# Kernel tuning notes

Hardware: AMD Instinct MI355X
Metric: run time of the kernel (lower is better)

## Reference

```python
import jax, jax.numpy as jnp
import numpy as np

C_I, C_T, NUM_HEADS = 128, 256, 8
EPS = 1e-5

def conv3d1(x, W, b):
    # 1x1x1 conv: x (b,c,D,H,W), W (o,c), b (o,)
    return jnp.einsum('oc,bcdhw->bodhw', W, x) + b[None, :, None, None, None]

def conv1d1(x, W, b):
    # kernel_size=1 conv: x (b,c,l), W (o,c), b (o,)
    return jnp.einsum('oc,bcl->bol', W, x) + b[None, :, None]

def inorm3d(x):
    # InstanceNorm3d(affine=False): normalize over spatial dims, biased var
    m = jnp.mean(x, axis=(2, 3, 4), keepdims=True)
    v = jnp.var(x, axis=(2, 3, 4), keepdims=True)
    return (x - m) * jax.lax.rsqrt(v + EPS)

def setup_inputs() -> dict:
    key = jax.random.key(0)
    ks = jax.random.split(key, 20)
    B, D, H, W, L = 2, 48, 48, 48, 20
    s = 0.05
    inp = {
        'img_in': jax.random.normal(ks[0], (B, C_I, D, H, W), jnp.float32),
        'lang_in': jax.random.normal(ks[1], (B, C_T, L), jnp.float32),
        'Wq': jax.random.normal(ks[2], (C_I, C_I), jnp.float32) * s,
        'bq': jnp.zeros((C_I,), jnp.float32),
        'Wk': jax.random.normal(ks[3], (C_I, C_T), jnp.float32) * s,
        'bk': jnp.zeros((C_I,), jnp.float32),
        'Wv': jax.random.normal(ks[4], (C_I, C_T), jnp.float32) * s,
        'bv': jnp.zeros((C_I,), jnp.float32),
        'Wpw': jax.random.normal(ks[5], (C_I, C_I), jnp.float32) * s,
        'bpw': jnp.zeros((C_I,), jnp.float32),
        'Wpi': jax.random.normal(ks[6], (C_I, C_I), jnp.float32) * s,
        'bpi': jnp.zeros((C_I,), jnp.float32),
        'Wpo': jax.random.normal(ks[7], (C_I, C_I), jnp.float32) * s,
        'bpo': jnp.zeros((C_I,), jnp.float32),
        'Wg1': jax.random.normal(ks[8], (C_I, C_I), jnp.float32) * s,
        'bg1': jnp.zeros((C_I,), jnp.float32),
        'Wg2': jax.random.normal(ks[9], (C_I, C_I), jnp.float32) * s,
        'bg2': jnp.zeros((C_I,), jnp.float32),
    }
    return inp

def reference(img_in, lang_in, Wq, bq, Wk, bk, Wv, bv, Wpw, bpw, Wpi, bpi,
              Wpo, bpo, Wg1, bg1, Wg2, bg2):
    b = img_in.shape[0]
    d = int(np.prod(img_in.shape[-3:]))
    l = lang_in.shape[-1]
    hd = C_I // NUM_HEADS
    # lang_mask=None path -> all-ones mask (additive term is zero but kept faithful)
    mask = jnp.ones((b, 1, l), img_in.dtype)

    # query: conv3d(1x1)+InstanceNorm -> (b, heads, d, hd)
    q = inorm3d(conv3d1(img_in, Wq, bq)).reshape(b, C_I, d)
    q = q.transpose(0, 2, 1).reshape(b, d, NUM_HEADS, hd).transpose(0, 2, 1, 3)
    # key/value: conv1d(k=1) masked -> (b, heads, hd, l)
    k = (conv1d1(lang_in, Wk, bk) * mask).reshape(b, NUM_HEADS, hd, l)
    v = (conv1d1(lang_in, Wv, bv) * mask).reshape(b, NUM_HEADS, hd, l)

    scale = (C_I / NUM_HEADS) ** (-0.5)
    sim = jnp.einsum('bhdc,bhcl->bhdl', q, k) * scale
    sim = sim + (10000.0 * mask[:, :, None, :] - 10000.0)  # (b,1,1,l) broadcast
    attn = jax.nn.softmax(sim, axis=-1)
    x = jnp.einsum('bhdl,bhcl->bhdc', attn, v)              # (b,heads,d,hd)
    x = x.transpose(0, 2, 1, 3).reshape(b, d, C_I)
    # faithful to torch .permute(0,2,1).permute(0,2,1).view_as(img_in):
    # reshape (b, d, c_i) flat buffer into (b, c_i, D, H, W)
    x_img = x.reshape(img_in.shape)

    skip = inorm3d(conv3d1(img_in, Wpi, bpi))
    weight = inorm3d(conv3d1(x_img, Wpw, bpw))
    out = jax.nn.relu(conv3d1(skip * weight, Wpo, bpo))
    gate = jnp.tanh(conv3d1(jax.nn.relu(conv3d1(out, Wg1, bg1)), Wg2, bg2))
    return out * gate
```

## Files before the change

kernel.cpp:

```cpp
#include <hip/hip_runtime.h>
#include <cstdint>
#include <cstddef>

#define PSP 110592
#define NCH 128
#define NB  2
#define CPW 68
#define TPB 4
static constexpr float EPSV = 1e-5f;

typedef short bf16x8 __attribute__((ext_vector_type(8)));
typedef float f32x4  __attribute__((ext_vector_type(4)));

static __device__ __forceinline__ short f2bf(float f) {
    uint32_t u = __builtin_bit_cast(uint32_t, f);
    u += 0x7FFF + ((u >> 16) & 1);
    return (short)(u >> 16);
}
static __device__ __forceinline__ float bf2f(short s) {
    uint32_t u = ((uint32_t)(uint16_t)s) << 16;
    return __builtin_bit_cast(float, u);
}
static __device__ __forceinline__ float bfLO(uint32_t w) { return bf2f((short)(w & 0xffff)); }
static __device__ __forceinline__ float bfHI(uint32_t w) { return bf2f((short)(w >> 16)); }
static __device__ __forceinline__ uint32_t pk2f(float lo, float hi) {
    return (uint32_t)(uint16_t)f2bf(lo) | ((uint32_t)(uint16_t)f2bf(hi) << 16);
}
static __device__ __forceinline__ uint32_t pk2s(short lo, short hi) {
    return (uint32_t)(uint16_t)lo | ((uint32_t)(uint16_t)hi << 16);
}
static __device__ __forceinline__ int swzb(int p) {
    return (((p & 7) ^ ((p >> 3) & 7)) << 4);
}

__global__ __launch_bounds__(256) void kv_kernel(
    const float* __restrict__ lang,
    const float* __restrict__ Wk, const float* __restrict__ bk,
    const float* __restrict__ Wv, const float* __restrict__ bv,
    float* __restrict__ kout, float* __restrict__ vout)
{
    int gid = blockIdx.x * 256 + threadIdx.x;
    int sel = gid / 5120;
    int r   = gid % 5120;
    int b   = r / 2560;
    int o   = (r % 2560) / 20;
    int l   = r % 20;
    const float* W  = sel ? Wv : Wk;
    const float* bb = sel ? bv : bk;
    const float* lg = lang + b * 256 * 20 + l;
    float acc = bb[o];
    #pragma unroll 8
    for (int c = 0; c < 256; ++c)
        acc = fmaf(W[o * 256 + c], lg[c * 20], acc);
    (sel ? vout : kout)[b * 2560 + o * 20 + l] = acc;
}

__global__ __launch_bounds__(256) void wprep_kernel(
    const float* __restrict__ w0, const float* __restrict__ w1,
    const float* __restrict__ w2, const float* __restrict__ w3,
    const float* __restrict__ w4, const float* __restrict__ w5,
    short* __restrict__ wt)
{
    const int m = blockIdx.x >> 4, s = blockIdx.x & 15;
    const float* src = w0;
    if (m == 1) src = w1; else if (m == 2) src = w2; else if (m == 3) src = w3;
    else if (m == 4) src = w4; else if (m == 5) src = w5;
    short* dst = wt + m * NCH * NCH;
    const int i0 = s * 1024 + threadIdx.x * 4;
    f32x4 v = *(const f32x4*)(src + i0);
    *(uint2*)(dst + i0) = make_uint2(pk2f(v[0], v[1]) ,
                                     pk2f(v[2], v[3]));
}

__global__ __launch_bounds__(256) void knprep_kernel(
    const float* __restrict__ qs, const float* __restrict__ qs2,
    const float* __restrict__ kbuf,
    float* __restrict__ knb, float* __restrict__ cbb)
{
    __shared__ float mq[128], rqs[128], knl[2560];
    const int t = threadIdx.x, b = blockIdx.x;
    if (t < 128) {
        float m = qs[b * 128 + t] * (1.0f / PSP);
        float v = qs2[b * 128 + t] * (1.0f / PSP) - m * m;
        mq[t] = m;
        rqs[t] = rsqrtf(v + EPSV) * 0.25f;
    }
    __syncthreads();
    for (int e = t; e < 2560; e += 256) {
        int c = e / 20;
        float kv = rqs[c] * kbuf[b * 2560 + e];
        knl[e] = kv;
        knb[b * 2560 + e] = kv;
    }
    __syncthreads();
    if (t < 160) {
        int h = t / 20, l = t % 20;
        float s = 0.0f;
        #pragma unroll
        for (int i = 0; i < 16; ++i)
            s = fmaf(mq[h * 16 + i], knl[(h * 16 + i) * 20 + l], s);
        cbb[b * 160 + t] = s;
    }
}

struct PackW { uint32_t lo[8], hi[8]; };

static __device__ __forceinline__ void ldpack_f32(const float* src, PackW& w) {
    const int t = threadIdx.x;
    const float* s = src + (size_t)(4 * (t >> 3)) * PSP + (t & 7) * 8;
    f32x4 r0a = *(const f32x4*)s,             r0b = *(const f32x4*)(s + 4);
    f32x4 r1a = *(const f32x4*)(s + PSP),     r1b = *(const f32x4*)(s + PSP + 4);
    f32x4 r2a = *(const f32x4*)(s + 2 * PSP), r2b = *(const f32x4*)(s + 2 * PSP + 4);
    f32x4 r3a = *(const f32x4*)(s + 3 * PSP), r3b = *(const f32x4*)(s + 3 * PSP + 4);
    #pragma unroll
    for (int j = 0; j < 4; ++j) {
        w.lo[j]     = pk2f(r0a[j], r1a[j]);
        w.lo[4 + j] = pk2f(r0b[j], r1b[j]);
        w.hi[j]     = pk2f(r2a[j], r3a[j]);
        w.hi[4 + j] = pk2f(r2b[j], r3b[j]);
    }
}
static __device__ __forceinline__ void ldpack_b16(const short* src, PackW& w) {
    const int t = threadIdx.x;
    const short* s = src + (size_t)(4 * (t >> 3)) * PSP + (t & 7) * 8;
    bf16x8 r0 = *(const bf16x8*)s;
    bf16x8 r1 = *(const bf16x8*)(s + PSP);
    bf16x8 r2 = *(const bf16x8*)(s + 2 * PSP);
    bf16x8 r3 = *(const bf16x8*)(s + 3 * PSP);
    #pragma unroll
    for (int j = 0; j < 8; ++j) { w.lo[j] = pk2s(r0[j], r1[j]); w.hi[j] = pk2s(r2[j], r3[j]); }
}
static __device__ __forceinline__ void ldpack_g4(const short* skip, const short* wgt,
        const float nm[4][NCH], PackW& w) {
    const int t = threadIdx.x;
    const int c = 4 * (t >> 3), p0 = (t & 7) * 8;
    const short* s = skip + (size_t)c * PSP + p0;
    const short* g = wgt  + (size_t)c * PSP + p0;
    bf16x8 s0 = *(const bf16x8*)s,             s1 = *(const bf16x8*)(s + PSP);
    bf16x8 s2 = *(const bf16x8*)(s + 2 * PSP), s3 = *(const bf16x8*)(s + 3 * PSP);
    bf16x8 g0 = *(const bf16x8*)g,             g1 = *(const bf16x8*)(g + PSP);
    bf16x8 g2 = *(const bf16x8*)(g + 2 * PSP), g3 = *(const bf16x8*)(g + 3 * PSP);
    float mA[4], rA[4], mB[4], rB[4];
    #pragma unroll
    for (int r = 0; r < 4; ++r) {
        mA[r] = nm[0][c + r]; rA[r] = nm[1][c + r];
        mB[r] = nm[2][c + r]; rB[r] = nm[3][c + r];
    }
    #pragma unroll
    for (int j = 0; j < 8; ++j) {
        float v0 = ((bf2f(s0[j]) - mA[0]) * rA[0]) * ((bf2f(g0[j]) - mB[0]) * rB[0]);
        float v1 = ((bf2f(s1[j]) - mA[1]) * rA[1]) * ((bf2f(g1[j]) - mB[1]) * rB[1]);
        float v2 = ((bf2f(s2[j]) - mA[2]) * rA[2]) * ((bf2f(g2[j]) - mB[2]) * rB[2]);
        float v3 = ((bf2f(s3[j]) - mA[3]) * rA[3]) * ((bf2f(g3[j]) - mB[3]) * rB[3]);
        w.lo[j] = pk2f(v0, v1);
        w.hi[j] = pk2f(v2, v3);
    }
}
static __device__ __forceinline__ void stage(char* STGb, const PackW& w) {
    const int t = threadIdx.x;
    const int c8 = (t >> 3) * 8, p0 = (t & 7) * 8;
    #pragma unroll
    for (int j = 0; j < 8; ++j) {
        int byte = (p0 + j) * 256 + c8;
        byte ^= ((j ^ (t & 7)) << 4);
        *(uint2*)(STGb + byte) = make_uint2(w.lo[j], w.hi[j]);
    }
}

static __device__ __forceinline__ void load_afrag16(const short* __restrict__ W16,
                                                    int wid, int lane, bf16x8 af[2][4]) {
    const int orow = wid * 32 + (lane & 15);
    const int cb   = (lane >> 4) * 8;
    #pragma unroll
    for (int mt = 0; mt < 2; ++mt)
        #pragma unroll
        for (int kt = 0; kt < 4; ++kt)
            af[mt][kt] = *(const bf16x8*)(W16 + (size_t)(orow + mt * 16) * NCH + kt * 32 + cb);
}

static __device__ __forceinline__ void run_mfmaX(const char* STGb, const bf16x8 af[2][4],
                                                 f32x4 acc[2][4], int lane) {
    const int l15 = lane & 15, kh = lane >> 4;
    #pragma unroll
    for (int nt = 0; nt < 4; ++nt) {
        const int p = nt * 16 + l15;
        const int sw = swzb(p);
        bf16x8 bf[4];
        #pragma unroll
        for (int kt = 0; kt < 4; ++kt)
            bf[kt] = *(const bf16x8*)(STGb + ((p * 256 + kt * 64 + kh * 16) ^ sw));
        #pragma unroll
        for (int kt = 0; kt < 4; ++kt) {
            acc[0][nt] = __builtin_amdgcn_mfma_f32_16x16x32_bf16(af[0][kt], bf[kt], acc[0][nt], 0, 0, 0);
            acc[1][nt] = __builtin_amdgcn_mfma_f32_16x16x32_bf16(af[1][kt], bf[kt], acc[1][nt], 0, 0, 0);
        }
    }
}
static __device__ __forceinline__ void zero_acc(f32x4 acc[2][4]) {
    #pragma unroll
    for (int m = 0; m < 2; ++m)
        #pragma unroll
        for (int n = 0; n < 4; ++n) acc[m][n] = (f32x4)0.0f;
}
static __device__ __forceinline__ void write_LCp(uint32_t* LCp, const f32x4 acc[2][4],
                                                 int wid, int lane) {
    const int l15 = lane & 15, og = wid * 32 + (lane >> 4) * 4;
    #pragma unroll
    for (int mt = 0; mt < 2; ++mt)
        #pragma unroll
        for (int nt = 0; nt < 4; ++nt) {
            const int o2 = (og >> 1) + mt * 8, p = nt * 16 + l15;
            f32x4 a = acc[mt][nt];
            LCp[o2 * CPW + p]       = pk2f(a[0], a[1]);
            LCp[(o2 + 1) * CPW + p] = pk2f(a[2], a[3]);
        }
}
template<bool RELU, bool STATS>
static __device__ __forceinline__ void epi2(const uint32_t* LCp, const float* __restrict__ bias,
        short* __restrict__ dst, float sS[4], float sQ[4])
{
    const int t = threadIdx.x;
    #pragma unroll
    for (int r = 0; r < 4; ++r) {
        const int u = r * 256 + t, o = u >> 3, ch = u & 7, hi = o & 1;
        const float bia = bias[o];
        const uint32_t* src = LCp + (o >> 1) * CPW + ch * 8;
        uint4 wa = *(const uint4*)src;
        uint4 wb = *(const uint4*)(src + 4);
        uint32_t ww[8] = {wa.x, wa.y, wa.z, wa.w, wb.x, wb.y, wb.z, wb.w};
        float v[8];
        #pragma unroll
        for (int j = 0; j < 8; ++j) v[j] = (hi ? bfHI(ww[j]) : bfLO(ww[j])) + bia;
        if (RELU) {
            #pragma unroll
            for (int j = 0; j < 8; ++j) v[j] = fmaxf(v[j], 0.0f);
        }
        bf16x8 s8;
        #pragma unroll
        for (int j = 0; j < 8; ++j) s8[j] = f2bf(v[j]);
        *(bf16x8*)(dst + (size_t)o * PSP + ch * 8) = s8;
        if (STATS) {
            float s = 0.0f, q = 0.0f;
            #pragma unroll
            for (int j = 0; j < 8; ++j) { s += v[j]; q += v[j] * v[j]; }
            sS[r] += s; sQ[r] += q;
        }
    }
}
static __device__ __forceinline__ void flush_stats(const float sS[4], const float sQ[4],
        float* __restrict__ s_sum, float* __restrict__ s_sq)
{
    const int t = threadIdx.x;
    #pragma unroll
    for (int r = 0; r < 4; ++r) {
        float s = sS[r], q = sQ[r];
        s += __shfl_xor(s, 1); q += __shfl_xor(q, 1);
        s += __shfl_xor(s, 2); q += __shfl_xor(q, 2);
        s += __shfl_xor(s, 4); q += __shfl_xor(q, 4);
        if ((t & 7) == 0) {
            atomicAdd(&s_sum[r * 32 + (t >> 3)], s);
            atomicAdd(&s_sq [r * 32 + (t >> 3)], q);
        }
    }
}

__global__ __launch_bounds__(256) void g12_kernel(
    const float* __restrict__ img, const short* __restrict__ w16,
    const float* __restrict__ bq, const float* __restrict__ bpi,
    short* __restrict__ qout, short* __restrict__ sout,
    float* __restrict__ qs, float* __restrict__ qs2,
    float* __restrict__ ss, float* __restrict__ ss2)
{
    __shared__ __align__(16) char STGb[16384];
    __shared__ __align__(16) uint32_t LCp[64 * CPW];

    const int t = threadIdx.x, lane = t & 63, wid = t >> 6;
    const int b = blockIdx.y;
    const size_t bbase = (size_t)b * NCH * PSP;
    const int pbase = blockIdx.x * (64 * TPB);
    const int sb = b * NCH;

    bf16x8 afq[2][4], afp[2][4];
    load_afrag16(w16, wid, lane, afq);
    load_afrag16(w16 + NCH * NCH, wid, lane, afp);

    float qS[4] = {0, 0, 0, 0}, qQ[4] = {0, 0, 0, 0};
    float sS[4] = {0, 0, 0, 0}, sQ[4] = {0, 0, 0, 0};

    PackW w;
    ldpack_f32(img + bbase + pbase, w);

    for (int i = 0; i < TPB; ++i) {
        const int pblk = pbase + i * 64;
        stage(STGb, w);
        __syncthreads();
        if (i + 1 < TPB) ldpack_f32(img + bbase + pblk + 64, w);
        f32x4 acc[2][4];
        zero_acc(acc);
        run_mfmaX(STGb, afq, acc, lane);
        write_LCp(LCp, acc, wid, lane);
        __syncthreads();
        epi2<false, true>(LCp, bq, qout + bbase + pblk, qS, qQ);
        zero_acc(acc);
        run_mfmaX(STGb, afp, acc, lane);
        __syncthreads();
        write_LCp(LCp, acc, wid, lane);
        __syncthreads();
        epi2<false, true>(LCp, bpi, sout + bbase + pblk, sS, sQ);
    }
    flush_stats(qS, qQ, qs + sb, qs2 + sb);
    flush_stats(sS, sQ, ss + sb, ss2 + sb);
}

__global__ __launch_bounds__(256) void g3_kernel(
    const short* __restrict__ x, const short* __restrict__ w16,
    const float* __restrict__ bpw, short* __restrict__ wout,
    float* __restrict__ wsu, float* __restrict__ ws2)
{
    __shared__ __align__(16) char STGb[16384];
    __shared__ __align__(16) uint32_t LCp[64 * CPW];

    const int t = threadIdx.x, lane = t & 63, wid = t >> 6;
    const int b = blockIdx.y;
    const size_t bbase = (size_t)b * NCH * PSP;
    const int pbase = blockIdx.x * (64 * TPB);
    const int sb = b * NCH;

    bf16x8 af[2][4];
    load_afrag16(w16, wid, lane, af);
    float wS[4] = {0, 0, 0, 0}, wQ[4] = {0, 0, 0, 0};

    PackW w;
    ldpack_b16(x + bbase + pbase, w);

    for (int i = 0; i < TPB; ++i) {
        const int pblk = pbase + i * 64;
        stage(STGb, w);
        __syncthreads();
        if (i + 1 < TPB) ldpack_b16(x + bbase + pblk + 64, w);
        f32x4 acc[2][4];
        zero_acc(acc);
        run_mfmaX(STGb, af, acc, lane);
        write_LCp(LCp, acc, wid, lane);
        __syncthreads();
        epi2<false, true>(LCp, bpw, wout + bbase + pblk, wS, wQ);
    }
    flush_stats(wS, wQ, wsu + sb, ws2 + sb);
}

__global__ __launch_bounds__(256) void g4_kernel(
    const short* __restrict__ skip, const short* __restrict__ wgt,
    const float* __restrict__ sA, const float* __restrict__ sA2,
    const float* __restrict__ sB, const float* __restrict__ sB2,
    const short* __restrict__ w16, const float* __restrict__ bpo,
    short* __restrict__ outp)
{
    __shared__ __align__(16) char STGb[16384];
    __shared__ __align__(16) uint32_t LCp[64 * CPW];
    __shared__ float nm[4][NCH];

    const int t = threadIdx.x, lane = t & 63, wid = t >> 6;
    const int b = blockIdx.y;
    const size_t bbase = (size_t)b * NCH * PSP;
    const int pbase = blockIdx.x * (64 * TPB);

    if (t < NCH) {
        float m = sA[b * NCH + t] * (1.0f / PSP);
        float v = sA2[b * NCH + t] * (1.0f / PSP) - m * m;
        nm[0][t] = m; nm[1][t] = rsqrtf(v + EPSV);
    } else {
        int c = t - NCH;
        float m = sB[b * NCH + c] * (1.0f / PSP);
        float v = sB2[b * NCH + c] * (1.0f / PSP) - m * m;
        nm[2][c] = m; nm[3][c] = rsqrtf(v + EPSV);
    }
    bf16x8 af[2][4];
    load_afrag16(w16, wid, lane, af);
    __syncthreads();

    PackW w;
    ldpack_g4(skip + bbase + pbase, wgt + bbase + pbase, nm, w);
    float dS[4], dQ[4];

    for (int i = 0; i < TPB; ++i) {
        const int pblk = pbase + i * 64;
        stage(STGb, w);
        __syncthreads();
        if (i + 1 < TPB)
            ldpack_g4(skip + bbase + pblk + 64, wgt + bbase + pblk + 64, nm, w);
        f32x4 acc[2][4];
        zero_acc(acc);
        run_mfmaX(STGb, af, acc, lane);
        write_LCp(LCp, acc, wid, lane);
        __syncthreads();
        epi2<true, false>(LCp, bpo, outp + bbase + pblk, dS, dQ);
    }
}

__global__ __launch_bounds__(256) void g56_kernel(
    const short* __restrict__ outb, const short* __restrict__ w16g1,
    const float* __restrict__ bg1, const short* __restrict__ w16g2,
    const float* __restrict__ bg2, float* __restrict__ fin)
{
    __shared__ __align__(16) char STGb[16384];
    __shared__ __align__(16) char RTL[64 * CPW * 4];

    const int t = threadIdx.x, lane = t & 63, wid = t >> 6;
    const int b = blockIdx.y;
    const size_t bbase = (size_t)b * NCH * PSP;
    const int pbase = blockIdx.x * (64 * TPB);

    bf16x8 af1[2][4], af2[2][4];
    load_afrag16(w16g1, wid, lane, af1);
    load_afrag16(w16g2, wid, lane, af2);

    float bg1v[2][4];
    {
        const int og = wid * 32 + (lane >> 4) * 4;
        #pragma unroll
        for (int mt = 0; mt < 2; ++mt)
            #pragma unroll
            for (int r = 0; r < 4; ++r) bg1v[mt][r] = bg1[og + mt * 16 + r];
    }

    PackW w;
    ldpack_b16(outb + bbase + pbase, w);

    for (int i = 0; i < TPB; ++i) {
        const int pblk = pbase + i * 64;
        stage(STGb, w);
        __syncthreads();
        if (i + 1 < TPB) ldpack_b16(outb + bbase + pblk + 64, w);
        f32x4 acc[2][4];
        zero_acc(acc);
        run_mfmaX(STGb, af1, acc, lane);
        {
            const int l15 = lane & 15, og = wid * 32 + (lane >> 4) * 4;
            #pragma unroll
            for (int mt = 0; mt < 2; ++mt)
                #pragma unroll
                for (int nt = 0; nt < 4; ++nt) {
                    const int o = og + mt * 16, p = nt * 16 + l15;
                    const int sw = swzb(p);
                    f32x4 a = acc[mt][nt];
                    float z0 = fmaxf(a[0] + bg1v[mt][0], 0.0f);
                    float z1 = fmaxf(a[1] + bg1v[mt][1], 0.0f);
                    float z2 = fmaxf(a[2] + bg1v[mt][2], 0.0f);
                    float z3 = fmaxf(a[3] + bg1v[mt][3], 0.0f);
                    *(uint32_t*)(RTL + ((p * 256 + o * 2) ^ sw))     = pk2f(z0, z1);
                    *(uint32_t*)(RTL + ((p * 256 + o * 2 + 4) ^ sw)) = pk2f(z2, z3);
                }
        }
        __syncthreads();
        zero_acc(acc);
        run_mfmaX(RTL, af2, acc, lane);
        __syncthreads();
        write_LCp((uint32_t*)RTL, acc, wid, lane);
        __syncthreads();
        {
            const uint32_t* LCp = (const uint32_t*)RTL;
            float* dst = fin + bbase + pblk;
            #pragma unroll
            for (int r = 0; r < 4; ++r) {
                const int u = r * 256 + t, o2 = u >> 4, ch = u & 15;
                const float b0 = bg2[2 * o2], b1 = bg2[2 * o2 + 1];
                uint4 lc = *(const uint4*)(LCp + o2 * CPW + ch * 4);
                uint32_t lw[4] = {lc.x, lc.y, lc.z, lc.w};
                f32x4 oA, oB;
                #pragma unroll
                for (int j = 0; j < 4; ++j) {
                    const int p = ch * 4 + j;
                    uint32_t mw = *(const uint32_t*)(STGb + ((p * 256 + o2 * 4) ^ swzb(p)));
                    oA[j] = bfLO(mw) * tanhf(bfLO(lw[j]) + b0);
                    oB[j] = bfHI(mw) * tanhf(bfHI(lw[j]) + b1);
                }
                *(f32x4*)(dst + (size_t)(2 * o2) * PSP + ch * 4)     = oA;
                *(f32x4*)(dst + (size_t)(2 * o2 + 1) * PSP + ch * 4) = oB;
            }
        }
        __syncthreads();
    }
}

__global__ __launch_bounds__(256) void attn3_kernel(
    const short* __restrict__ qpre, const float* __restrict__ knb,
    const float* __restrict__ cbb, const float* __restrict__ vbuf,
    short* __restrict__ xout)
{
    __shared__ __align__(16) uint32_t QX[64 * 65];
    __shared__ float KN[2560], VV[2560], CB[160];

    const int t = threadIdx.x;
    const int b = blockIdx.y;
    const int pblk = blockIdx.x * 64;
    const size_t bbase = (size_t)b * NCH * PSP;

    {
        const float* kn = knb + b * 2560;
        const float* vv = vbuf + b * 2560;
        #pragma unroll
        for (int e = t; e < 2560; e += 256) { KN[e] = kn[e]; VV[e] = vv[e]; }
        if (t < 160) CB[t] = cbb[b * 160 + t];
    }
    {
        const int c2 = t >> 2, p0 = (t & 3) * 16;
        const short* s0 = qpre + bbase + (size_t)(2 * c2) * PSP + pblk + p0;
        bf16x8 a0 = *(const bf16x8*)s0,         a1 = *(const bf16x8*)(s0 + 8);
        bf16x8 b0 = *(const bf16x8*)(s0 + PSP), b1 = *(const bf16x8*)(s0 + PSP + 8);
        uint32_t w[16];
        #pragma unroll
        for (int k = 0; k < 8; ++k) { w[k] = pk2s(a0[k], b0[k]); w[8 + k] = pk2s(a1[k], b1[k]); }
        uint32_t* base = QX + c2 * 65 + p0;
        #pragma unroll
        for (int k = 0; k < 8; ++k) *(uint2*)(base + 2 * k) = make_uint2(w[2 * k], w[2 * k + 1]);
    }
    __syncthreads();

    const int p = t & 63, h0 = t >> 6;
    uint32_t qw[16];
    #pragma unroll
    for (int i = 0; i < 8; ++i) {
        qw[i]     = QX[(h0 * 8 + i) * 65 + p];
        qw[8 + i] = QX[((h0 + 4) * 8 + i) * 65 + p];
    }
    __syncthreads();

    #pragma unroll 1
    for (int hh = 0; hh < 2; ++hh) {
        const int h = h0 + hh * 4;
        const int c0 = h * 16;
        float sim[20];
        #pragma unroll
        for (int l = 0; l < 20; ++l) sim[l] = -CB[h * 20 + l];
        #pragma unroll
        for (int i = 0; i < 8; ++i) {
            const uint32_t w = qw[hh * 8 + i];
            const float qlo = bfLO(w), qhi = bfHI(w);
            const float* k0 = KN + (c0 + 2 * i) * 20;
            #pragma unroll
            for (int l = 0; l < 20; ++l)
                sim[l] = fmaf(qlo, k0[l], fmaf(qhi, k0[20 + l], sim[l]));
        }
        float mx = sim[0];
        #pragma unroll
        for (int l = 1; l < 20; ++l) mx = fmaxf(mx, sim[l]);
        float se = 0.0f;
        #pragma unroll
        for (int l = 0; l < 20; ++l) { float e = __expf(sim[l] - mx); sim[l] = e; se += e; }
        const float inv = 1.0f / se;
        #pragma unroll
        for (int i = 0; i < 8; ++i) {
            const float* v0 = VV + (c0 + 2 * i) * 20;
            float x0 = 0.0f, x1 = 0.0f;
            #pragma unroll
            for (int l = 0; l < 20; ++l) {
                x0 = fmaf(sim[l], v0[l], x0);
                x1 = fmaf(sim[l], v0[20 + l], x1);
            }
            QX[p * 65 + h * 8 + i] = pk2f(x0 * inv, x1 * inv);
        }
    }
    __syncthreads();

    {
        const int lane = t & 63, w = t >> 6;
        uint32_t* gdst = (uint32_t*)(xout + bbase + (size_t)pblk * NCH);
        #pragma unroll
        for (int j = 0; j < 4; ++j) {
            const int pp = w * 4 + j * 16 + (lane >> 4);
            const int cw = (lane & 15) * 4;
            const uint32_t* s = QX + pp * 65 + cw;
            *(uint4*)(gdst + pp * 64 + cw) = make_uint4(s[0], s[1], s[2], s[3]);
        }
    }
}

extern "C" void kernel_launch(void* const* d_in, const int* in_sizes, int n_in,
                              void* d_out, int out_size, void* d_ws, size_t ws_size,
                              hipStream_t stream)
{
    const float* img  = (const float*)d_in[0];
    const float* lang = (const float*)d_in[1];
    const float* Wq   = (const float*)d_in[2];
    const float* bq   = (const float*)d_in[3];
    const float* Wk   = (const float*)d_in[4];
    const float* bk   = (const float*)d_in[5];
    const float* Wv   = (const float*)d_in[6];
    const float* bv   = (const float*)d_in[7];
    const float* Wpw  = (const float*)d_in[8];
    const float* bpw  = (const float*)d_in[9];
    const float* Wpi  = (const float*)d_in[10];
    const float* bpi  = (const float*)d_in[11];
    const float* Wpo  = (const float*)d_in[12];
    const float* bpo  = (const float*)d_in[13];
    const float* Wg1  = (const float*)d_in[14];
    const float* bg1  = (const float*)d_in[15];
    const float* Wg2  = (const float*)d_in[16];
    const float* bg2  = (const float*)d_in[17];
    float* outp = (float*)d_out;

    const size_t N = (size_t)NB * NCH * PSP;
    const size_t needed = 3 * N * sizeof(short) + 6 * NCH * NCH * sizeof(short)
                        + (3 * 2 * 2560 + 2 * 160 + 6 * 256) * sizeof(float);
    if (ws_size < needed) return;

    short* bufA = (short*)d_ws;
    short* bufB = bufA + N;
    short* bufC = bufB + N;
    short* wt16 = bufC + N;
    float* kbuf = (float*)(wt16 + 6 * NCH * NCH);
    float* vbuf = kbuf + 2 * 2560;
    float* knb  = vbuf + 2 * 2560;
    float* cbb  = knb + 2 * 2560;
    float* st   = cbb + 2 * 160;
    float* qs   = st;
    float* qs2  = st + 256;
    float* ss   = st + 512;
    float* ss2  = st + 768;
    float* wsu  = st + 1024;
    float* ws2  = st + 1280;

    hipMemsetAsync(st, 0, 6 * 256 * sizeof(float), stream);
    kv_kernel<<<dim3(40), dim3(256), 0, stream>>>(lang, Wk, bk, Wv, bv, kbuf, vbuf);
    wprep_kernel<<<dim3(96), dim3(256), 0, stream>>>(Wq, Wpi, Wpw, Wpo, Wg1, Wg2, wt16);

    const dim3 gg(PSP / (64 * TPB), NB), gb(256);

    g12_kernel<<<gg, gb, 0, stream>>>(img, wt16, bq, bpi, bufA, bufC, qs, qs2, ss, ss2);
    knprep_kernel<<<dim3(NB), dim3(256), 0, stream>>>(qs, qs2, kbuf, knb, cbb);
    attn3_kernel<<<dim3(PSP / 64, NB), gb, 0, stream>>>(bufA, knb, cbb, vbuf, bufB);
    g3_kernel<<<gg, gb, 0, stream>>>(bufB, wt16 + 2 * NCH * NCH, bpw, bufA, wsu, ws2);
    g4_kernel<<<gg, gb, 0, stream>>>(bufC, bufA, ss, ss2, wsu, ws2,
                                     wt16 + 3 * NCH * NCH, bpo, bufB);
    g56_kernel<<<gg, gb, 0, stream>>>(bufB, wt16 + 4 * NCH * NCH, bg1,
                                      wt16 + 5 * NCH * NCH, bg2, outp);
}
```

Baseline: 322.2 us.

## Store Q position-major, simplify attention kernel, repack loads, use hardware bf16 conversion

The q projection is now written in position-major (pixel x channel) layout straight from the g12 epilogue through a swizzled LDS tile, with stats computed in registers. The attention kernel then reads each pixel's 128-channel row directly, one thread per pixel, and drops the LDS transpose. Input packing switches to 8-channel by 4-position loads with byte-perm packing and uint4 LDS stores, bf16 conversion uses the packed intrinsic, and the norm is folded into scale/shift FMAs. TPB is halved, which doubles the block count and repeats weight-fragment loads more often.

New measurement: 430.8 us. +33.7%, slower.

```diff
diff --git a/kernel.cpp b/kernel.cpp
--- a/kernel.cpp
+++ b/kernel.cpp
@@ -1,4 +1,5 @@
 #include <hip/hip_runtime.h>
+#include <hip/hip_bf16.h>
 #include <cstdint>
 #include <cstddef>
 
@@ -6,28 +7,23 @@
 #define NCH 128
 #define NB  2
 #define CPW 68
-#define TPB 4
+#define TPB 2
 static constexpr float EPSV = 1e-5f;
 
 typedef short bf16x8 __attribute__((ext_vector_type(8)));
 typedef float f32x4  __attribute__((ext_vector_type(4)));
 
-static __device__ __forceinline__ short f2bf(float f) {
-    uint32_t u = __builtin_bit_cast(uint32_t, f);
-    u += 0x7FFF + ((u >> 16) & 1);
-    return (short)(u >> 16);
-}
-static __device__ __forceinline__ float bf2f(short s) {
-    uint32_t u = ((uint32_t)(uint16_t)s) << 16;
-    return __builtin_bit_cast(float, u);
-}
-static __device__ __forceinline__ float bfLO(uint32_t w) { return bf2f((short)(w & 0xffff)); }
-static __device__ __forceinline__ float bfHI(uint32_t w) { return bf2f((short)(w >> 16)); }
-static __device__ __forceinline__ uint32_t pk2f(float lo, float hi) {
-    return (uint32_t)(uint16_t)f2bf(lo) | ((uint32_t)(uint16_t)f2bf(hi) << 16);
-}
-static __device__ __forceinline__ uint32_t pk2s(short lo, short hi) {
-    return (uint32_t)(uint16_t)lo | ((uint32_t)(uint16_t)hi << 16);
+static __device__ __forceinline__ uint32_t cvtpk(float lo, float hi) {
+    __hip_bfloat162 h = __float22bfloat162_rn(make_float2(lo, hi));
+    uint32_t u;
+    __builtin_memcpy(&u, &h, 4);
+    return u;
+}
+static __device__ __forceinline__ float bfLO(uint32_t w) {
+    return __builtin_bit_cast(float, w << 16);
+}
+static __device__ __forceinline__ float bfHI(uint32_t w) {
+    return __builtin_bit_cast(float, w & 0xffff0000u);
 }
 static __device__ __forceinline__ int swzb(int p) {
     return (((p & 7) ^ ((p >> 3) & 7)) << 4);
@@ -68,8 +64,7 @@
     short* dst = wt + m * NCH * NCH;
     const int i0 = s * 1024 + threadIdx.x * 4;
     f32x4 v = *(const f32x4*)(src + i0);
-    *(uint2*)(dst + i0) = make_uint2(pk2f(v[0], v[1]) ,
-                                     pk2f(v[2], v[3]));
+    *(uint2*)(dst + i0) = make_uint2(cvtpk(v[0], v[1]), cvtpk(v[2], v[3]));
 }
 
 __global__ __launch_bounds__(256) void knprep_kernel(
@@ -103,67 +98,82 @@
     }
 }
 
-struct PackW { uint32_t lo[8], hi[8]; };
-
-static __device__ __forceinline__ void ldpack_f32(const float* src, PackW& w) {
+struct PackR { uint32_t r[4][4]; };
+
+static __device__ __forceinline__ void ldpack_f32(const float* src, PackR& w) {
     const int t = threadIdx.x;
-    const float* s = src + (size_t)(4 * (t >> 3)) * PSP + (t & 7) * 8;
-    f32x4 r0a = *(const f32x4*)s,             r0b = *(const f32x4*)(s + 4);
-    f32x4 r1a = *(const f32x4*)(s + PSP),     r1b = *(const f32x4*)(s + PSP + 4);
-    f32x4 r2a = *(const f32x4*)(s + 2 * PSP), r2b = *(const f32x4*)(s + 2 * PSP + 4);
-    f32x4 r3a = *(const f32x4*)(s + 3 * PSP), r3b = *(const f32x4*)(s + 3 * PSP + 4);
+    const float* s = src + (size_t)((t >> 4) * 8) * PSP + (t & 15) * 4;
+    f32x4 F[8];
+    #pragma unroll
+    for (int r = 0; r < 8; ++r) F[r] = *(const f32x4*)(s + (size_t)r * PSP);
+    #pragma unroll
+    for (int j = 0; j < 4; ++j)
+        #pragma unroll
+        for (int k = 0; k < 4; ++k)
+            w.r[j][k] = cvtpk(F[2 * k][j], F[2 * k + 1][j]);
+}
+static __device__ __forceinline__ void ldpack_b16(const short* src, PackR& w) {
+    const int t = threadIdx.x;
+    const short* s = src + (size_t)((t >> 4) * 8) * PSP + (t & 15) * 4;
+    uint2 L[8];
+    #pragma unroll
+    for (int r = 0; r < 8; ++r) L[r] = *(const uint2*)(s + (size_t)r * PSP);
     #pragma unroll
     for (int j = 0; j < 4; ++j) {
-        w.lo[j]     = pk2f(r0a[j], r1a[j]);
-        w.lo[4 + j] = pk2f(r0b[j], r1b[j]);
-        w.hi[j]     = pk2f(r2a[j], r3a[j]);
-        w.hi[4 + j] = pk2f(r2b[j], r3b[j]);
-    }
-}
-static __device__ __forceinline__ void ldpack_b16(const short* src, PackW& w) {
+        const uint32_t sel = (j & 1) ? 0x07060302u : 0x05040100u;
+        #pragma unroll
+        for (int k = 0; k < 4; ++k) {
+            uint32_t wa = (j & 2) ? L[2 * k].y : L[2 * k].x;
+            uint32_t wb = (j & 2) ? L[2 * k + 1].y : L[2 * k + 1].x;
+            w.r[j][k] = __builtin_amdgcn_perm(wb, wa, sel);
+        }
+    }
+}
+static __device__ __forceinline__ void ldpack_g4(const short* skip, const short* wgt,
+        const float nm[4][NCH], PackR& w) {
     const int t = threadIdx.x;
-    const short* s = src + (size_t)(4 * (t >> 3)) * PSP + (t & 7) * 8;
-    bf16x8 r0 = *(const bf16x8*)s;
-    bf16x8 r1 = *(const bf16x8*)(s + PSP);
-    bf16x8 r2 = *(const bf16x8*)(s + 2 * PSP);
-    bf16x8 r3 = *(const bf16x8*)(s + 3 * PSP);
-    #pragma unroll
-    for (int j = 0; j < 8; ++j) { w.lo[j] = pk2s(r0[j], r1[j]); w.hi[j] = pk2s(r2[j], r3[j]); }
-}
-static __device__ __forceinline__ void ldpack_g4(const short* skip, const short* wgt,
-        const float nm[4][NCH], PackW& w) {
+    const int c0 = (t >> 4) * 8, p0 = (t & 15) * 4;
+    const short* s = skip + (size_t)c0 * PSP + p0;
+    const short* g = wgt  + (size_t)c0 * PSP + p0;
+    uint2 LS[8], LG[8];
+    #pragma unroll
+    for (int r = 0; r < 8; ++r) {
+        LS[r] = *(const uint2*)(s + (size_t)r * PSP);
+        LG[r] = *(const uint2*)(g + (size_t)r * PSP);
+    }
+    float rA[8], tA[8], rB[8], tB[8];
+    #pragma unroll
+    for (int r = 0; r < 8; ++r) {
+        rA[r] = nm[0][c0 + r]; tA[r] = nm[1][c0 + r];
+        rB[r] = nm[2][c0 + r]; tB[r] = nm[3][c0 + r];
+    }
+    #pragma unroll
+    for (int j = 0; j < 4; ++j) {
+        #pragma unroll
+        for (int k = 0; k < 4; ++k) {
+            uint32_t wa = (j & 2) ? LS[2 * k].y : LS[2 * k].x;
+            uint32_t wb = (j & 2) ? LS[2 * k + 1].y : LS[2 * k + 1].x;
+            uint32_t ga = (j & 2) ? LG[2 * k].y : LG[2 * k].x;
+            uint32_t gb = (j & 2) ? LG[2 * k + 1].y : LG[2 * k + 1].x;
+            float s0 = (j & 1) ? bfHI(wa) : bfLO(wa);
+            float s1 = (j & 1) ? bfHI(wb) : bfLO(wb);
+            float g0 = (j & 1) ? bfHI(ga) : bfLO(ga);
+            float g1 = (j & 1) ? bfHI(gb) : bfLO(gb);
+            float v0 = fmaf(s0, rA[2 * k], tA[2 * k]) * fmaf(g0, rB[2 * k], tB[2 * k]);
+            float v1 = fmaf(s1, rA[2 * k + 1], tA[2 * k + 1]) * fmaf(g1, rB[2 * k + 1], tB[2 * k + 1]);
+            w.r[j][k] = cvtpk(v0, v1);
+        }
+    }
+}
+static __device__ __forceinline__ void stage(char* STGb, const PackR& w) {
     const int t = threadIdx.x;
-    const int c = 4 * (t >> 3), p0 = (t & 7) * 8;
-    const short* s = skip + (size_t)c * PSP + p0;
-    const short* g = wgt  + (size_t)c * PSP + p0;
-    bf16x8 s0 = *(const bf16x8*)s,             s1 = *(const bf16x8*)(s + PSP);
-    bf16x8 s2 = *(const bf16x8*)(s + 2 * PSP), s3 = *(const bf16x8*)(s + 3 * PSP);
-    bf16x8 g0 = *(const bf16x8*)g,             g1 = *(const bf16x8*)(g + PSP);
-    bf16x8 g2 = *(const bf16x8*)(g + 2 * PSP), g3 = *(const bf16x8*)(g + 3 * PSP);
-    float mA[4], rA[4], mB[4], rB[4];
-    #pragma unroll
-    for (int r = 0; r < 4; ++r) {
-        mA[r] = nm[0][c + r]; rA[r] = nm[1][c + r];
-        mB[r] = nm[2][c + r]; rB[r] = nm[3][c + r];
-    }
-    #pragma unroll
-    for (int j = 0; j < 8; ++j) {
-        float v0 = ((bf2f(s0[j]) - mA[0]) * rA[0]) * ((bf2f(g0[j]) - mB[0]) * rB[0]);
-        float v1 = ((bf2f(s1[j]) - mA[1]) * rA[1]) * ((bf2f(g1[j]) - mB[1]) * rB[1]);
-        float v2 = ((bf2f(s2[j]) - mA[2]) * rA[2]) * ((bf2f(g2[j]) - mB[2]) * rB[2]);
-        float v3 = ((bf2f(s3[j]) - mA[3]) * rA[3]) * ((bf2f(g3[j]) - mB[3]) * rB[3]);
-        w.lo[j] = pk2f(v0, v1);
-        w.hi[j] = pk2f(v2, v3);
-    }
-}
-static __device__ __forceinline__ void stage(char* STGb, const PackW& w) {
-    const int t = threadIdx.x;
-    const int c8 = (t >> 3) * 8, p0 = (t & 7) * 8;
-    #pragma unroll
-    for (int j = 0; j < 8; ++j) {
-        int byte = (p0 + j) * 256 + c8;
-        byte ^= ((j ^ (t & 7)) << 4);
-        *(uint2*)(STGb + byte) = make_uint2(w.lo[j], w.hi[j]);
+    const int cB = (t >> 4) * 16, p0 = (t & 15) * 4;
+    #pragma unroll
+    for (int j = 0; j < 4; ++j) {
+        const int p = p0 + j;
+        int byte = p * 256 + cB;
+        byte ^= swzb(p);
+        *(uint4*)(STGb + byte) = make_uint4(w.r[j][0], w.r[j][1], w.r[j][2], w.r[j][3]);
     }
 }
 
@@ -177,7 +187,6 @@
         for (int kt = 0; kt < 4; ++kt)
             af[mt][kt] = *(const bf16x8*)(W16 + (size_t)(orow + mt * 16) * NCH + kt * 32 + cb);
 }
-
 static __device__ __forceinline__ void run_mfmaX(const char* STGb, const bf16x8 af[2][4],
                                                  f32x4 acc[2][4], int lane) {
     const int l15 = lane & 15, kh = lane >> 4;
@@ -211,8 +220,8 @@
         for (int nt = 0; nt < 4; ++nt) {
             const int o2 = (og >> 1) + mt * 8, p = nt * 16 + l15;
             f32x4 a = acc[mt][nt];
-            LCp[o2 * CPW + p]       = pk2f(a[0], a[1]);
-            LCp[(o2 + 1) * CPW + p] = pk2f(a[2], a[3]);
+            LCp[o2 * CPW + p]       = cvtpk(a[0], a[1]);
+            LCp[(o2 + 1) * CPW + p] = cvtpk(a[2], a[3]);
         }
 }
 template<bool RELU, bool STATS>
@@ -235,10 +244,9 @@
             #pragma unroll
             for (int j = 0; j < 8; ++j) v[j] = fmaxf(v[j], 0.0f);
         }
-        bf16x8 s8;
-        #pragma unroll
-        for (int j = 0; j < 8; ++j) s8[j] = f2bf(v[j]);
-        *(bf16x8*)(dst + (size_t)o * PSP + ch * 8) = s8;
+        *(uint4*)(dst + (size_t)o * PSP + ch * 8) =
+            make_uint4(cvtpk(v[0], v[1]), cvtpk(v[2], v[3]),
+                       cvtpk(v[4], v[5]), cvtpk(v[6], v[7]));
         if (STATS) {
             float s = 0.0f, q = 0.0f;
             #pragma unroll
@@ -267,9 +275,101 @@
 __global__ __launch_bounds__(256) void g12_kernel(
     const float* __restrict__ img, const short* __restrict__ w16,
     const float* __restrict__ bq, const float* __restrict__ bpi,
-    short* __restrict__ qout, short* __restrict__ sout,
+    short* __restrict__ qpm, short* __restrict__ sout,
     float* __restrict__ qs, float* __restrict__ qs2,
     float* __restrict__ ss, float* __restrict__ ss2)
+{
+    __shared__ __align__(16) char STGb[16384];
+    __shared__ __align__(16) char LC[64 * CPW * 4];
+
+    const int t = threadIdx.x, lane = t & 63, wid = t >> 6;
+    const int b = blockIdx.y;
+    const size_t bbase = (size_t)b * NCH * PSP;
+    const size_t bpos  = (size_t)b * PSP;
+    const int pbase = blockIdx.x * (64 * TPB);
+    const int sb = b * NCH;
+
+    bf16x8 afq[2][4], afp[2][4];
+    load_afrag16(w16, wid, lane, afq);
+    load_afrag16(w16 + NCH * NCH, wid, lane, afp);
+
+    const int og0 = wid * 32 + (lane >> 4) * 4;
+    float bqv[2][4];
+    #pragma unroll
+    for (int mt = 0; mt < 2; ++mt)
+        #pragma unroll
+        for (int r = 0; r < 4; ++r) bqv[mt][r] = bq[og0 + mt * 16 + r];
+
+    float qS[2][4] = {{0,0,0,0},{0,0,0,0}}, qQ[2][4] = {{0,0,0,0},{0,0,0,0}};
+    float sS[4] = {0,0,0,0}, sQ[4] = {0,0,0,0};
+
+    PackR w;
+    ldpack_f32(img + bbase + pbase, w);
+
+    for (int i = 0; i < TPB; ++i) {
+        const int pblk = pbase + i * 64;
+        stage(STGb, w);
+        __syncthreads();
+        if (i + 1 < TPB) ldpack_f32(img + bbase + pblk + 64, w);
+        f32x4 acc[2][4];
+        zero_acc(acc);
+        run_mfmaX(STGb, afq, acc, lane);
+        {
+            const int l15 = lane & 15;
+            #pragma unroll
+            for (int mt = 0; mt < 2; ++mt)
+                #pragma unroll
+                for (int nt = 0; nt < 4; ++nt) {
+                    const int o = og0 + mt * 16, p = nt * 16 + l15, sw = swzb(p);
+                    f32x4 a = acc[mt][nt];
+                    float v0 = a[0] + bqv[mt][0], v1 = a[1] + bqv[mt][1];
+                    float v2 = a[2] + bqv[mt][2], v3 = a[3] + bqv[mt][3];
+                    *(uint32_t*)(LC + ((p * 256 + o * 2)     ^ sw)) = cvtpk(v0, v1);
+                    *(uint32_t*)(LC + ((p * 256 + o * 2 + 4) ^ sw)) = cvtpk(v2, v3);
+                    qS[mt][0] += v0; qS[mt][1] += v1; qS[mt][2] += v2; qS[mt][3] += v3;
+                    qQ[mt][0] += v0 * v0; qQ[mt][1] += v1 * v1;
+                    qQ[mt][2] += v2 * v2; qQ[mt][3] += v3 * v3;
+                }
+        }
+        __syncthreads();
+        {
+            const int p = t >> 2, cq = t & 3;
+            const int sw = swzb(p);
+            short* qdst = qpm + (size_t)(bpos + pblk + p) * 128 + cq * 32;
+            #pragma unroll
+            for (int k = 0; k < 4; ++k) {
+                uint4 d = *(const uint4*)(LC + ((p * 256 + cq * 64 + k * 16) ^ sw));
+                *(uint4*)(qdst + k * 8) = d;
+            }
+        }
+        zero_acc(acc);
+        run_mfmaX(STGb, afp, acc, lane);
+        __syncthreads();
+        write_LCp((uint32_t*)LC, acc, wid, lane);
+        __syncthreads();
+        epi2<false, true>((const uint32_t*)LC, bpi, sout + bbase + pblk, sS, sQ);
+    }
+    #pragma unroll
+    for (int mt = 0; mt < 2; ++mt)
+        #pragma unroll
+        for (int r = 0; r < 4; ++r) {
+            float s = qS[mt][r], q = qQ[mt][r];
+            s += __shfl_xor(s, 1); q += __shfl_xor(q, 1);
+            s += __shfl_xor(s, 2); q += __shfl_xor(q, 2);
+            s += __shfl_xor(s, 4); q += __shfl_xor(q, 4);
+            s += __shfl_xor(s, 8); q += __shfl_xor(q, 8);
+            if ((lane & 15) == 0) {
+                atomicAdd(&qs [sb + og0 + mt * 16 + r], s);
+                atomicAdd(&qs2[sb + og0 + mt * 16 + r], q);
+            }
+        }
+    flush_stats(sS, sQ, ss + sb, ss2 + sb);
+}
+
+__global__ __launch_bounds__(256) void g3_kernel(
+    const short* __restrict__ x, const short* __restrict__ w16,
+    const float* __restrict__ bpw, short* __restrict__ wout,
+    float* __restrict__ wsu, float* __restrict__ ws2)
 {
     __shared__ __align__(16) char STGb[16384];
     __shared__ __align__(16) uint32_t LCp[64 * CPW];
@@ -280,57 +380,11 @@
     const int pbase = blockIdx.x * (64 * TPB);
     const int sb = b * NCH;
 
-    bf16x8 afq[2][4], afp[2][4];
-    load_afrag16(w16, wid, lane, afq);
-    load_afrag16(w16 + NCH * NCH, wid, lane, afp);
-
-    float qS[4] = {0, 0, 0, 0}, qQ[4] = {0, 0, 0, 0};
-    float sS[4] = {0, 0, 0, 0}, sQ[4] = {0, 0, 0, 0};
-
-    PackW w;
-    ldpack_f32(img + bbase + pbase, w);
-
-    for (int i = 0; i < TPB; ++i) {
-        const int pblk = pbase + i * 64;
-        stage(STGb, w);
-        __syncthreads();
-        if (i + 1 < TPB) ldpack_f32(img + bbase + pblk + 64, w);
-        f32x4 acc[2][4];
-        zero_acc(acc);
-        run_mfmaX(STGb, afq, acc, lane);
-        write_LCp(LCp, acc, wid, lane);
-        __syncthreads();
-        epi2<false, true>(LCp, bq, qout + bbase + pblk, qS, qQ);
-        zero_acc(acc);
-        run_mfmaX(STGb, afp, acc, lane);
-        __syncthreads();
-        write_LCp(LCp, acc, wid, lane);
-        __syncthreads();
-        epi2<false, true>(LCp, bpi, sout + bbase + pblk, sS, sQ);
-    }
-    flush_stats(qS, qQ, qs + sb, qs2 + sb);
-    flush_stats(sS, sQ, ss + sb, ss2 + sb);
-}
-
-__global__ __launch_bounds__(256) void g3_kernel(
-    const short* __restrict__ x, const short* __restrict__ w16,
-    const float* __restrict__ bpw, short* __restrict__ wout,
-    float* __restrict__ wsu, float* __restrict__ ws2)
-{
-    __shared__ __align__(16) char STGb[16384];
-    __shared__ __align__(16) uint32_t LCp[64 * CPW];
-
-    const int t = threadIdx.x, lane = t & 63, wid = t >> 6;
-    const int b = blockIdx.y;
-    const size_t bbase = (size_t)b * NCH * PSP;
-    const int pbase = blockIdx.x * (64 * TPB);
-    const int sb = b * NCH;
-
     bf16x8 af[2][4];
     load_afrag16(w16, wid, lane, af);
-    float wS[4] = {0, 0, 0, 0}, wQ[4] = {0, 0, 0, 0};
-
-    PackW w;
+    float wS[4] = {0,0,0,0}, wQ[4] = {0,0,0,0};
+
+    PackR w;
     ldpack_b16(x + bbase + pbase, w);
 
     for (int i = 0; i < TPB; ++i) {
@@ -367,20 +421,22 @@
     if (t < NCH) {
         float m = sA[b * NCH + t] * (1.0f / PSP);
         float v = sA2[b * NCH + t] * (1.0f / PSP) - m * m;
-        nm[0][t] = m; nm[1][t] = rsqrtf(v + EPSV);
+        float r = rsqrtf(v + EPSV);
+        nm[0][t] = r; nm[1][t] = -m * r;
     } else {
         int c = t - NCH;
         float m = sB[b * NCH + c] * (1.0f / PSP);
         float v = sB2[b * NCH + c] * (1.0f / PSP) - m * m;
-        nm[2][c] = m; nm[3][c] = rsqrtf(v + EPSV);
+        float r = rsqrtf(v + EPSV);
+        nm[2][c] = r; nm[3][c] = -m * r;
     }
     bf16x8 af[2][4];
     load_afrag16(w16, wid, lane, af);
     __syncthreads();
 
-    PackW w;
+    float dS[4], dQ[4];
+    PackR w;
     ldpack_g4(skip + bbase + pbase, wgt + bbase + pbase, nm, w);
-    float dS[4], dQ[4];
 
     for (int i = 0; i < TPB; ++i) {
         const int pblk = pbase + i * 64;
@@ -423,7 +479,7 @@
             for (int r = 0; r < 4; ++r) bg1v[mt][r] = bg1[og + mt * 16 + r];
     }
 
-    PackW w;
+    PackR w;
     ldpack_b16(outb + bbase + pbase, w);
 
     for (int i = 0; i < TPB; ++i) {
@@ -447,8 +503,8 @@
                     float z1 = fmaxf(a[1] + bg1v[mt][1], 0.0f);
                     float z2 = fmaxf(a[2] + bg1v[mt][2], 0.0f);
                     float z3 = fmaxf(a[3] + bg1v[mt][3], 0.0f);
-                    *(uint32_t*)(RTL + ((p * 256 + o * 2) ^ sw))     = pk2f(z0, z1);
-                    *(uint32_t*)(RTL + ((p * 256 + o * 2 + 4) ^ sw)) = pk2f(z2, z3);
+                    *(uint32_t*)(RTL + ((p * 256 + o * 2)     ^ sw)) = cvtpk(z0, z1);
+                    *(uint32_t*)(RTL + ((p * 256 + o * 2 + 4) ^ sw)) = cvtpk(z2, z3);
                 }
         }
         __syncthreads();
@@ -482,61 +538,40 @@
     }
 }
 
-__global__ __launch_bounds__(256) void attn3_kernel(
-    const short* __restrict__ qpre, const float* __restrict__ knb,
+__global__ __launch_bounds__(256) void attn4_kernel(
+    const short* __restrict__ qpm, const float* __restrict__ knb,
     const float* __restrict__ cbb, const float* __restrict__ vbuf,
     short* __restrict__ xout)
 {
-    __shared__ __align__(16) uint32_t QX[64 * 65];
     __shared__ float KN[2560], VV[2560], CB[160];
-
     const int t = threadIdx.x;
     const int b = blockIdx.y;
-    const int pblk = blockIdx.x * 64;
-    const size_t bbase = (size_t)b * NCH * PSP;
+    const size_t bpos = (size_t)b * PSP;
+    const int p = blockIdx.x * 256 + t;
 
     {
         const float* kn = knb + b * 2560;
         const float* vv = vbuf + b * 2560;
-        #pragma unroll
         for (int e = t; e < 2560; e += 256) { KN[e] = kn[e]; VV[e] = vv[e]; }
         if (t < 160) CB[t] = cbb[b * 160 + t];
     }
-    {
-        const int c2 = t >> 2, p0 = (t & 3) * 16;
-        const short* s0 = qpre + bbase + (size_t)(2 * c2) * PSP + pblk + p0;
-        bf16x8 a0 = *(const bf16x8*)s0,         a1 = *(const bf16x8*)(s0 + 8);
-        bf16x8 b0 = *(const bf16x8*)(s0 + PSP), b1 = *(const bf16x8*)(s0 + PSP + 8);
-        uint32_t w[16];
-        #pragma unroll
-        for (int k = 0; k < 8; ++k) { w[k] = pk2s(a0[k], b0[k]); w[8 + k] = pk2s(a1[k], b1[k]); }
-        uint32_t* base = QX + c2 * 65 + p0;
-        #pragma unroll
-        for (int k = 0; k < 8; ++k) *(uint2*)(base + 2 * k) = make_uint2(w[2 * k], w[2 * k + 1]);
-    }
     __syncthreads();
 
-    const int p = t & 63, h0 = t >> 6;
-    uint32_t qw[16];
-    #pragma unroll
-    for (int i = 0; i < 8; ++i) {
-        qw[i]     = QX[(h0 * 8 + i) * 65 + p];
-        qw[8 + i] = QX[((h0 + 4) * 8 + i) * 65 + p];
-    }
-    __syncthreads();
+    const short* qrow = qpm + (bpos + p) * 128;
+    short* xrow = xout + (bpos + p) * 128;
 
     #pragma unroll 1
-    for (int hh = 0; hh < 2; ++hh) {
-        const int h = h0 + hh * 4;
-        const int c0 = h * 16;
+    for (int h = 0; h < 8; ++h) {
+        uint4 qa = *(const uint4*)(qrow + h * 16);
+        uint4 qb = *(const uint4*)(qrow + h * 16 + 8);
+        uint32_t qu[8] = {qa.x, qa.y, qa.z, qa.w, qb.x, qb.y, qb.z, qb.w};
         float sim[20];
         #pragma unroll
         for (int l = 0; l < 20; ++l) sim[l] = -CB[h * 20 + l];
         #pragma unroll
         for (int i = 0; i < 8; ++i) {
-            const uint32_t w = qw[hh * 8 + i];
-            const float qlo = bfLO(w), qhi = bfHI(w);
-            const float* k0 = KN + (c0 + 2 * i) * 20;
+            const float qlo = bfLO(qu[i]), qhi = bfHI(qu[i]);
+            const float* k0 = KN + (h * 16 + 2 * i) * 20;
             #pragma unroll
             for (int l = 0; l < 20; ++l)
                 sim[l] = fmaf(qlo, k0[l], fmaf(qhi, k0[20 + l], sim[l]));
@@ -548,30 +583,20 @@
         #pragma unroll
         for (int l = 0; l < 20; ++l) { float e = __expf(sim[l] - mx); sim[l] = e; se += e; }
         const float inv = 1.0f / se;
+        uint32_t xu[8];
         #pragma unroll
         for (int i = 0; i < 8; ++i) {
-            const float* v0 = VV + (c0 + 2 * i) * 20;
+            const float* v0 = VV + (h * 16 + 2 * i) * 20;
             float x0 = 0.0f, x1 = 0.0f;
             #pragma unroll
             for (int l = 0; l < 20; ++l) {
                 x0 = fmaf(sim[l], v0[l], x0);
                 x1 = fmaf(sim[l], v0[20 + l], x1);
             }
-            QX[p * 65 + h * 8 + i] = pk2f(x0 * inv, x1 * inv);
-        }
-    }
-    __syncthreads();
-
-    {
-        const int lane = t & 63, w = t >> 6;
-        uint32_t* gdst = (uint32_t*)(xout + bbase + (size_t)pblk * NCH);
-        #pragma unroll
-        for (int j = 0; j < 4; ++j) {
-            const int pp = w * 4 + j * 16 + (lane >> 4);
-            const int cw = (lane & 15) * 4;
-            const uint32_t* s = QX + pp * 65 + cw;
-            *(uint4*)(gdst + pp * 64 + cw) = make_uint4(s[0], s[1], s[2], s[3]);
-        }
+            xu[i] = cvtpk(x0 * inv, x1 * inv);
+        }
+        *(uint4*)(xrow + h * 16)     = make_uint4(xu[0], xu[1], xu[2], xu[3]);
+        *(uint4*)(xrow + h * 16 + 8) = make_uint4(xu[4], xu[5], xu[6], xu[7]);
     }
 }
 
@@ -620,7 +645,7 @@
     float* wsu  = st + 1024;
     float* ws2  = st + 1280;
 
-    hipMemsetAsync(st, 0, 6 * 256 * sizeof(float), stream);
+    (void)hipMemsetAsync(st, 0, 6 * 256 * sizeof(float), stream);
     kv_kernel<<<dim3(40), dim3(256), 0, stream>>>(lang, Wk, bk, Wv, bv, kbuf, vbuf);
     wprep_kernel<<<dim3(96), dim3(256), 0, stream>>>(Wq, Wpi, Wpw, Wpo, Wg1, Wg2, wt16);
 
@@ -628,7 +653,7 @@
 
     g12_kernel<<<gg, gb, 0, stream>>>(img, wt16, bq, bpi, bufA, bufC, qs, qs2, ss, ss2);
     knprep_kernel<<<dim3(NB), dim3(256), 0, stream>>>(qs, qs2, kbuf, knb, cbb);
-    attn3_kernel<<<dim3(PSP / 64, NB), gb, 0, stream>>>(bufA, knb, cbb, vbuf, bufB);
+    attn4_kernel<<<dim3(PSP / 256, NB), gb, 0, stream>>>(bufA, knb, cbb, vbuf, bufB);
     g3_kernel<<<gg, gb, 0, stream>>>(bufB, wt16 + 2 * NCH * NCH, bpw, bufA, wsu, ws2);
     g4_kernel<<<gg, gb, 0, stream>>>(bufC, bufA, ss, ss2, wsu, ws2,
                                      wt16 + 3 * NCH * NCH, bpo, bufB);
```
